# Performance work log

Measured on AMD Instinct MI355X. Metric: run time of the kernel, lower is better.

The kernel has to match this reference:

```python
import jax, jax.numpy as jnp
import numpy as np

B, T, V, E, H, FC, O = 4096, 64, 512, 32, 128, 256, 1024


def setup_inputs() -> dict:
    key = jax.random.key(0)
    ks = jax.random.split(key, 12)
    n = lambda k, shape, sc=1.0: (jax.random.normal(k, shape, jnp.float32) * sc)
    return {
        "message": n(ks[0], (B, T, V), 0.1),
        "W_emb": n(ks[1], (E, V), 0.05),
        "b_emb": n(ks[2], (E,), 0.05),
        "init_emb": n(ks[3], (1, 1, E), 1.0),
        "W_ih": n(ks[4], (3 * H, E), 0.08),
        "W_hh": n(ks[5], (3 * H, H), 0.08),
        "b_ih": n(ks[6], (3 * H,), 0.05),
        "b_hh": n(ks[7], (3 * H,), 0.05),
        "W_fc1": n(ks[8], (FC, H), 0.08),
        "b_fc1": n(ks[9], (FC,), 0.05),
        "W_fc2": n(ks[10], (O, FC), 0.05),
        "b_fc2": n(ks[11], (O,), 0.05),
    }


def reference(message, W_emb, b_emb, init_emb, W_ih, W_hh, b_ih, b_hh,
              W_fc1, b_fc1, W_fc2, b_fc2):
    Bb, Tt, Vv = message.shape
    Hh = W_hh.shape[1]
    # Per-step embedding of the message (torch does this inside the loop;
    # it is a pure per-timestep linear so we batch it once): [B,T,E]
    emb = jnp.einsum('btv,ev->bte', message, W_emb) + b_emb
    # Inputs consumed by the GRU at step t: initial_embedding at t=0,
    # then embedding(message[:, t-1]) for t >= 1. The embedding of the
    # final token is computed in torch but never fed to the GRU.
    x0 = jnp.broadcast_to(init_emb[0], (Bb, init_emb.shape[-1]))  # [B,E]
    xs = jnp.concatenate([x0[:, None, :], emb[:, :Tt - 1, :]], axis=1)  # [B,T,E]
    # Precompute input-side gate pre-activations for all steps: [T,B,3H]
    gi_all = jnp.einsum('bte,ge->tbg', xs, W_ih) + b_ih

    def gru_step(h, gi):
        gh = h @ W_hh.T + b_hh  # [B,3H]
        i_r, i_z, i_n = jnp.split(gi, 3, axis=-1)
        h_r, h_z, h_n = jnp.split(gh, 3, axis=-1)
        r = jax.nn.sigmoid(i_r + h_r)
        z = jax.nn.sigmoid(i_z + h_z)
        nng = jnp.tanh(i_n + r * h_n)
        h_new = (1.0 - z) * nng + z * h
        return h_new, None

    h0 = jnp.zeros((Bb, Hh), message.dtype)
    h_last, _ = jax.lax.scan(gru_step, h0, gi_all)
    hid = jax.nn.elu(h_last @ W_fc1.T + b_fc1)
    return jax.nn.sigmoid(hid @ W_fc2.T + b_fc2)
```

## Files before the change

### kernel.cpp

```cpp
#include <hip/hip_runtime.h>
#include <math.h>

#define B_ 4096
#define T_ 64
#define V_ 512
#define E_ 32
#define H_ 128
#define FC1_ 256
#define O_ 1024

typedef float f32x4 __attribute__((ext_vector_type(4)));
typedef short s16x8 __attribute__((ext_vector_type(8)));
typedef unsigned short u16;

#define MFMA16(a, b, c) __builtin_amdgcn_mfma_f32_16x16x32_bf16(a, b, c, 0, 0, 0)

union Frag { u16 q[8]; unsigned u[4]; s16x8 v; };

__device__ __forceinline__ u16 f2bf(float f) {
    union { float f; unsigned u; } v; v.f = f;
    unsigned r = v.u + 0x7FFFu + ((v.u >> 16) & 1u);
    return (u16)(r >> 16);
}
__device__ __forceinline__ unsigned cvtpk(float lo, float hi) {
    unsigned r;
    asm("v_cvt_pk_bf16_f32 %0, %1, %2" : "=v"(r) : "v"(lo), "v"(hi));
    return r;
}
__device__ __forceinline__ float sigf(float x) { return 1.0f / (1.0f + __expf(-x)); }
__device__ __forceinline__ float tanhfast(float x) {
    return 1.0f - 2.0f / (__expf(2.0f * x) + 1.0f);
}
__device__ __forceinline__ s16x8 gatherB(const float* W, int row, int K, int k0, int lh) {
    const float* p = W + (size_t)row * K + k0 + lh * 8;
    float4 a = *(const float4*)p;
    float4 b = *(const float4*)(p + 4);
    Frag f;
    f.u[0] = cvtpk(a.x, a.y); f.u[1] = cvtpk(a.z, a.w);
    f.u[2] = cvtpk(b.x, b.y); f.u[3] = cvtpk(b.z, b.w);
    return f.v;
}

#define LDS_BARRIER() do {                                         \
    asm volatile("s_waitcnt lgkmcnt(0)" ::: "memory");             \
    __builtin_amdgcn_s_barrier();                                  \
} while (0)

__global__ void __launch_bounds__(512, 2) fused_kernel(
    const float* __restrict__ msg,
    const float* __restrict__ Wemb, const float* __restrict__ b_emb,
    const float* __restrict__ init_emb,
    const float* __restrict__ Wih, const float* __restrict__ Whh,
    const float* __restrict__ b_ih, const float* __restrict__ b_hh,
    const float* __restrict__ Wfc1, const float* __restrict__ b_fc1,
    const float* __restrict__ Wfc2, const float* __restrict__ b_fc2,
    float* __restrict__ out) {
    __shared__ float mlds[2][16][516];
    __shared__ u16 hlds[2][16 * 136];
    __shared__ float epart[2][8][576];
    __shared__ u16 xfrag[2][640];
    u16* const hidl = (u16*)&epart[0][0][0];
    const int tid = threadIdx.x, w = tid >> 6, l = tid & 63;
    const int ln = l & 15, lh = l >> 4;
    const int wg = w & 3, wp = w >> 2;
    const int gb = blockIdx.x;

#define LOADCOL(BUF, C) do {                                                   \
    _Pragma("unroll")                                                          \
    for (int i_ = 0; i_ < 4; i_++) {                                           \
        int r_ = 2 * w + (i_ >> 1);                                            \
        int o_ = (i_ & 1) * 256 + l * 4;                                       \
        BUF[i_] = *(const f32x4*)(msg +                                        \
            ((size_t)(gb * 16 + r_) * T_ + (C)) * V_ + o_);                    \
    }                                                                          \
} while (0)
#define WRITECOL(BUF, MB) do {                                                 \
    _Pragma("unroll")                                                          \
    for (int i_ = 0; i_ < 4; i_++) {                                           \
        int r_ = 2 * w + (i_ >> 1);                                            \
        int o_ = (i_ & 1) * 256 + l * 4;                                       \
        *(f32x4*)&mlds[MB][r_][o_] = BUF[i_];                                  \
    }                                                                          \
} while (0)

    f32x4 mb0[4], mb1[4], mb2[4], mb3[4];
    LOADCOL(mb0, 0); LOADCOL(mb1, 1); LOADCOL(mb2, 2); LOADCOL(mb3, 3);

    s16x8 wh[3][4], wi[3], we[2][2];
    float br, bz, bin, bgn;
    {
        #pragma unroll
        for (int g = 0; g < 3; g++) {
            int gt = wg + 4 * wp + 8 * g;
            #pragma unroll
            for (int kc = 0; kc < 4; kc++)
                wh[g][kc] = gatherB(Whh, gt * 16 + ln, 128, kc * 32, lh);
            wi[g] = gatherB(Wih, gt * 16 + ln, 32, 0, lh);
        }
        #pragma unroll
        for (int kk = 0; kk < 2; kk++) {
            we[kk][0] = gatherB(Wemb, ln, 512, (2 * w + kk) * 32, lh);
            we[kk][1] = gatherB(Wemb, 16 + ln, 512, (2 * w + kk) * 32, lh);
        }
        int c = wg * 16 + wp * 64 + ln;
        br  = b_ih[c] + b_hh[c];
        bz  = b_ih[128 + c] + b_hh[128 + c];
        bin = b_ih[256 + c];
        bgn = b_hh[256 + c];
    }
    const float bev = b_emb[tid & 31];
    float hold[4] = {};

    for (int i = tid; i < 16 * 136; i += 512) hlds[0][i] = 0;
    {
        int fr_ = tid >> 5, fc_ = tid & 31;
        xfrag[1][fr_ * 40 + fc_] = f2bf(init_emb[fc_]);
    }
    WRITECOL(mb0, 0);
    WRITECOL(mb1, 1);
    __syncthreads();

#define EMBED_LDS(BUF, PAR) do {                                               \
    f32x4 e0 = {0.f, 0.f, 0.f, 0.f}, e1 = {0.f, 0.f, 0.f, 0.f};                \
    _Pragma("unroll")                                                          \
    for (int kk = 0; kk < 2; kk++) {                                           \
        const float* mp = &mlds[BUF][ln][(2 * w + kk) * 32 + lh * 8];          \
        f32x4 m0 = *(const f32x4*)mp;                                          \
        f32x4 m1 = *(const f32x4*)(mp + 4);                                    \
        Frag fa;                                                               \
        fa.u[0] = cvtpk(m0[0], m0[1]); fa.u[1] = cvtpk(m0[2], m0[3]);          \
        fa.u[2] = cvtpk(m1[0], m1[1]); fa.u[3] = cvtpk(m1[2], m1[3]);          \
        e0 = MFMA16(fa.v, we[kk][0], e0);                                      \
        e1 = MFMA16(fa.v, we[kk][1], e1);                                      \
    }                                                                          \
    _Pragma("unroll")                                                          \
    for (int i = 0; i < 4; i++) {                                              \
        epart[PAR][w][(lh * 4 + i) * 36 + ln]      = e0[i];                    \
        epart[PAR][w][(lh * 4 + i) * 36 + 16 + ln] = e1[i];                    \
    }                                                                          \
} while (0)

    EMBED_LDS(0, 1);
    LDS_BARRIER();

    const int aoff = ln * 136 + lh * 8;
    const int colo = wg * 16 + wp * 64 + ln;
    const int fr = tid >> 5, fc = tid & 31, fo = fr * 36 + fc;

#define GRU_STEP(TT, K, LOADF, WRF, EMBF, REDF, MB_L, MB_W) do {               \
    const int t = (TT);                                                        \
    if (LOADF) LOADCOL(MB_L, t + 4);                                           \
    const u16* hb = hlds[(K) & 1];                                             \
    s16x8 af0 = *(const s16x8*)(hb + aoff);                                    \
    s16x8 af1 = *(const s16x8*)(hb + aoff + 32);                               \
    s16x8 af2 = *(const s16x8*)(hb + aoff + 64);                               \
    s16x8 af3 = *(const s16x8*)(hb + aoff + 96);                               \
    s16x8 xc = *(const s16x8*)(&xfrag[((K) + 1) & 1][0] + ln * 40 + lh * 8);   \
    f32x4 ar  = {br, br, br, br};                                              \
    f32x4 az  = {bz, bz, bz, bz};                                              \
    f32x4 agn = {bgn, bgn, bgn, bgn};                                          \
    f32x4 ain = {bin, bin, bin, bin};                                          \
    ar  = MFMA16(xc, wi[0], ar);                                               \
    az  = MFMA16(xc, wi[1], az);                                               \
    ain = MFMA16(xc, wi[2], ain);                                              \
    ar  = MFMA16(af0, wh[0][0], ar);                                           \
    ar  = MFMA16(af1, wh[0][1], ar);                                           \
    ar  = MFMA16(af2, wh[0][2], ar);                                           \
    ar  = MFMA16(af3, wh[0][3], ar);                                           \
    az  = MFMA16(af0, wh[1][0], az);                                           \
    az  = MFMA16(af1, wh[1][1], az);                                           \
    az  = MFMA16(af2, wh[1][2], az);                                           \
    az  = MFMA16(af3, wh[1][3], az);                                           \
    agn = MFMA16(af0, wh[2][0], agn);                                          \
    agn = MFMA16(af1, wh[2][1], agn);                                          \
    agn = MFMA16(af2, wh[2][2], agn);                                          \
    agn = MFMA16(af3, wh[2][3], agn);                                          \
    if (WRF) WRITECOL(MB_W, (K) & 1);                                          \
    u16* hw = hlds[((K) + 1) & 1];                                             \
    float hn[4];                                                               \
    _Pragma("unroll")                                                          \
    for (int i = 0; i < 4; i++) {                                              \
        float rg = sigf(ar[i]);                                                \
        float zg = sigf(az[i]);                                                \
        float ng = tanhfast(ain[i] + rg * agn[i]);                             \
        hn[i] = zg * (hold[i] - ng) + ng;                                      \
        hold[i] = hn[i];                                                       \
    }                                                                          \
    {                                                                          \
        unsigned u01 = cvtpk(hn[0], hn[1]);                                    \
        unsigned u23 = cvtpk(hn[2], hn[3]);                                    \
        hw[(lh * 4 + 0) * 136 + colo] = (u16)(u01 & 0xFFFFu);                  \
        hw[(lh * 4 + 1) * 136 + colo] = (u16)(u01 >> 16);                      \
        hw[(lh * 4 + 2) * 136 + colo] = (u16)(u23 & 0xFFFFu);                  \
        hw[(lh * 4 + 3) * 136 + colo] = (u16)(u23 >> 16);                      \
    }                                                                          \
    if (EMBF) EMBED_LDS(((K) + 1) & 1, (K) & 1);                               \
    if (REDF) {                                                                \
        const float* eb = &epart[((K) + 1) & 1][0][0];                         \
        float s = eb[fo]           + eb[576 + fo]     + eb[2 * 576 + fo]       \
                + eb[3 * 576 + fo] + eb[4 * 576 + fo] + eb[5 * 576 + fo]       \
                + eb[6 * 576 + fo] + eb[7 * 576 + fo] + bev;                   \
        xfrag[(K) & 1][fr * 40 + fc] = f2bf(s);                                \
    }                                                                          \
    LDS_BARRIER();                                                             \
} while (0)

    for (int tt = 0; tt < 60; tt += 4) {
        GRU_STEP(tt + 0, 0, 1, 1, 1, 1, mb0, mb2);
        GRU_STEP(tt + 1, 1, 1, 1, 1, 1, mb1, mb3);
        GRU_STEP(tt + 2, 2, 1, 1, 1, 1, mb2, mb0);
        GRU_STEP(tt + 3, 3, 1, 1, 1, 1, mb3, mb1);
    }
    GRU_STEP(60, 0, 0, 1, 1, 1, mb0, mb2);
    GRU_STEP(61, 1, 0, 1, 1, 1, mb1, mb3);
    GRU_STEP(62, 2, 0, 0, 1, 1, mb2, mb0);
    GRU_STEP(63, 3, 0, 0, 0, 0, mb3, mb1);
#undef GRU_STEP
#undef LOADCOL
#undef WRITECOL
#undef EMBED_LDS

    const u16* hb = hlds[0];
    s16x8 hf0 = *(const s16x8*)(hb + aoff);
    s16x8 hf1 = *(const s16x8*)(hb + aoff + 32);
    s16x8 hf2 = *(const s16x8*)(hb + aoff + 64);
    s16x8 hf3 = *(const s16x8*)(hb + aoff + 96);
    #pragma unroll
    for (int q = 0; q < 2; q++) {
        int ot = 2 * w + q;
        float b1 = b_fc1[ot * 16 + ln];
        f32x4 a1 = {b1, b1, b1, b1};
        a1 = MFMA16(hf0, gatherB(Wfc1, ot * 16 + ln, 128, 0,  lh), a1);
        a1 = MFMA16(hf1, gatherB(Wfc1, ot * 16 + ln, 128, 32, lh), a1);
        a1 = MFMA16(hf2, gatherB(Wfc1, ot * 16 + ln, 128, 64, lh), a1);
        a1 = MFMA16(hf3, gatherB(Wfc1, ot * 16 + ln, 128, 96, lh), a1);
        #pragma unroll
        for (int i = 0; i < 4; i++) {
            float v = a1[i];
            v = v > 0.0f ? v : (__expf(v) - 1.0f);
            hidl[(lh * 4 + i) * 264 + ot * 16 + ln] = f2bf(v);
        }
    }
    LDS_BARRIER();

    s16x8 hf[8];
    #pragma unroll
    for (int kc = 0; kc < 8; kc++)
        hf[kc] = *(const s16x8*)(hidl + ln * 264 + kc * 32 + lh * 8);
    #pragma unroll
    for (int q = 0; q < 8; q++) {
        int nt = 8 * w + q;
        float b2 = b_fc2[nt * 16 + ln];
        f32x4 a2 = {b2, b2, b2, b2};
        #pragma unroll
        for (int kc = 0; kc < 8; kc++)
            a2 = MFMA16(hf[kc], gatherB(Wfc2, nt * 16 + ln, 256, kc * 32, lh), a2);
        #pragma unroll
        for (int i = 0; i < 4; i++)
            out[(size_t)(gb * 16 + lh * 4 + i) * 1024 + nt * 16 + ln] = sigf(a2[i]);
    }
}

extern "C" void kernel_launch(void* const* d_in, const int* in_sizes, int n_in,
                              void* d_out, int out_size, void* d_ws, size_t ws_size,
                              hipStream_t stream) {
    const float* message  = (const float*)d_in[0];
    const float* W_emb    = (const float*)d_in[1];
    const float* b_emb    = (const float*)d_in[2];
    const float* init_emb = (const float*)d_in[3];
    const float* W_ih     = (const float*)d_in[4];
    const float* W_hh     = (const float*)d_in[5];
    const float* b_ih     = (const float*)d_in[6];
    const float* b_hh     = (const float*)d_in[7];
    const float* W_fc1    = (const float*)d_in[8];
    const float* b_fc1    = (const float*)d_in[9];
    const float* W_fc2    = (const float*)d_in[10];
    const float* b_fc2    = (const float*)d_in[11];
    float* out = (float*)d_out;
    (void)d_ws; (void)ws_size;

    hipLaunchKernelGGL(fused_kernel, dim3(256), dim3(512), 0, stream,
                       message, W_emb, b_emb, init_emb, W_ih, W_hh, b_ih, b_hh,
                       W_fc1, b_fc1, W_fc2, b_fc2, out);
}
```

Before: 161.3 us.

## Specialize four extra wavefronts as message loaders feeding LDS for GRU waves

Raises the block to 768 threads and dedicates the four extra wavefronts to streaming message columns from global memory into the LDS double buffer, two steps ahead. The eight original wavefronts now only run the embedding, GRU recurrence and output MLP, so they no longer issue global loads or hold prefetch registers. The aim is to take global-load latency and register pressure off the serial recurrence path. In exchange, the prefetch depth drops from four columns to two, and the launch bound of (768, 3) may force heavy register limits and spills on the compute wavefronts.

```diff
diff --git a/kernel.cpp b/kernel.cpp
--- a/kernel.cpp
+++ b/kernel.cpp
@@ -46,7 +46,7 @@
     __builtin_amdgcn_s_barrier();                                  \
 } while (0)
 
-__global__ void __launch_bounds__(512, 2) fused_kernel(
+__global__ void __launch_bounds__(768, 3) fused_kernel(
     const float* __restrict__ msg,
     const float* __restrict__ Wemb, const float* __restrict__ b_emb,
     const float* __restrict__ init_emb,
@@ -62,33 +62,39 @@
     u16* const hidl = (u16*)&epart[0][0][0];
     const int tid = threadIdx.x, w = tid >> 6, l = tid & 63;
     const int ln = l & 15, lh = l >> 4;
-    const int wg = w & 3, wp = w >> 2;
+    const int wg = w & 3, wp = (w >> 2) & 1;
     const int gb = blockIdx.x;
-
-#define LOADCOL(BUF, C) do {                                                   \
-    _Pragma("unroll")                                                          \
-    for (int i_ = 0; i_ < 4; i_++) {                                           \
-        int r_ = 2 * w + (i_ >> 1);                                            \
+    const bool isload = (w >= 8);
+    const int lw = w & 3;
+
+#define L_LOAD(BUF, C) do {                                                    \
+    _Pragma("unroll")                                                          \
+    for (int i_ = 0; i_ < 8; i_++) {                                           \
+        int r_ = 4 * lw + (i_ >> 1);                                           \
         int o_ = (i_ & 1) * 256 + l * 4;                                       \
         BUF[i_] = *(const f32x4*)(msg +                                        \
             ((size_t)(gb * 16 + r_) * T_ + (C)) * V_ + o_);                    \
     }                                                                          \
 } while (0)
-#define WRITECOL(BUF, MB) do {                                                 \
-    _Pragma("unroll")                                                          \
-    for (int i_ = 0; i_ < 4; i_++) {                                           \
-        int r_ = 2 * w + (i_ >> 1);                                            \
+#define L_WRITE(BUF, MB) do {                                                  \
+    _Pragma("unroll")                                                          \
+    for (int i_ = 0; i_ < 8; i_++) {                                           \
+        int r_ = 4 * lw + (i_ >> 1);                                           \
         int o_ = (i_ & 1) * 256 + l * 4;                                       \
         *(f32x4*)&mlds[MB][r_][o_] = BUF[i_];                                  \
     }                                                                          \
 } while (0)
 
-    f32x4 mb0[4], mb1[4], mb2[4], mb3[4];
-    LOADCOL(mb0, 0); LOADCOL(mb1, 1); LOADCOL(mb2, 2); LOADCOL(mb3, 3);
-
+    f32x4 lb0[8], lb1[8];
     s16x8 wh[3][4], wi[3], we[2][2];
-    float br, bz, bin, bgn;
-    {
+    float br = 0.f, bz = 0.f, bin = 0.f, bgn = 0.f, bev = 0.f;
+    float hold[4] = {};
+
+    if (isload) {
+        L_LOAD(lb0, 0); L_WRITE(lb0, 0);
+        L_LOAD(lb1, 1); L_WRITE(lb1, 1);
+        L_LOAD(lb0, 2); L_LOAD(lb1, 3);
+    } else {
         #pragma unroll
         for (int g = 0; g < 3; g++) {
             int gt = wg + 4 * wp + 8 * g;
@@ -107,17 +113,13 @@
         bz  = b_ih[128 + c] + b_hh[128 + c];
         bin = b_ih[256 + c];
         bgn = b_hh[256 + c];
-    }
-    const float bev = b_emb[tid & 31];
-    float hold[4] = {};
-
-    for (int i = tid; i < 16 * 136; i += 512) hlds[0][i] = 0;
-    {
+        bev = b_emb[tid & 31];
+    }
+    if (tid < 512) {
+        for (int i = tid; i < 16 * 136; i += 512) hlds[0][i] = 0;
         int fr_ = tid >> 5, fc_ = tid & 31;
         xfrag[1][fr_ * 40 + fc_] = f2bf(init_emb[fc_]);
     }
-    WRITECOL(mb0, 0);
-    WRITECOL(mb1, 1);
     __syncthreads();
 
 #define EMBED_LDS(BUF, PAR) do {                                               \
@@ -140,124 +142,131 @@
     }                                                                          \
 } while (0)
 
-    EMBED_LDS(0, 1);
+    if (!isload) EMBED_LDS(0, 1);
     LDS_BARRIER();
 
     const int aoff = ln * 136 + lh * 8;
     const int colo = wg * 16 + wp * 64 + ln;
     const int fr = tid >> 5, fc = tid & 31, fo = fr * 36 + fc;
 
-#define GRU_STEP(TT, K, LOADF, WRF, EMBF, REDF, MB_L, MB_W) do {               \
+#define STEP(TT, P, LOADF, WRF, EMBF, REDF, LB) do {                           \
     const int t = (TT);                                                        \
-    if (LOADF) LOADCOL(MB_L, t + 4);                                           \
-    const u16* hb = hlds[(K) & 1];                                             \
-    s16x8 af0 = *(const s16x8*)(hb + aoff);                                    \
-    s16x8 af1 = *(const s16x8*)(hb + aoff + 32);                               \
-    s16x8 af2 = *(const s16x8*)(hb + aoff + 64);                               \
-    s16x8 af3 = *(const s16x8*)(hb + aoff + 96);                               \
-    s16x8 xc = *(const s16x8*)(&xfrag[((K) + 1) & 1][0] + ln * 40 + lh * 8);   \
-    f32x4 ar  = {br, br, br, br};                                              \
-    f32x4 az  = {bz, bz, bz, bz};                                              \
-    f32x4 agn = {bgn, bgn, bgn, bgn};                                          \
-    f32x4 ain = {bin, bin, bin, bin};                                          \
-    ar  = MFMA16(xc, wi[0], ar);                                               \
-    az  = MFMA16(xc, wi[1], az);                                               \
-    ain = MFMA16(xc, wi[2], ain);                                              \
-    ar  = MFMA16(af0, wh[0][0], ar);                                           \
-    ar  = MFMA16(af1, wh[0][1], ar);                                           \
-    ar  = MFMA16(af2, wh[0][2], ar);                                           \
-    ar  = MFMA16(af3, wh[0][3], ar);                                           \
-    az  = MFMA16(af0, wh[1][0], az);                                           \
-    az  = MFMA16(af1, wh[1][1], az);                                           \
-    az  = MFMA16(af2, wh[1][2], az);                                           \
-    az  = MFMA16(af3, wh[1][3], az);                                           \
-    agn = MFMA16(af0, wh[2][0], agn);                                          \
-    agn = MFMA16(af1, wh[2][1], agn);                                          \
-    agn = MFMA16(af2, wh[2][2], agn);                                          \
-    agn = MFMA16(af3, wh[2][3], agn);                                          \
-    if (WRF) WRITECOL(MB_W, (K) & 1);                                          \
-    u16* hw = hlds[((K) + 1) & 1];                                             \
-    float hn[4];                                                               \
-    _Pragma("unroll")                                                          \
-    for (int i = 0; i < 4; i++) {                                              \
-        float rg = sigf(ar[i]);                                                \
-        float zg = sigf(az[i]);                                                \
-        float ng = tanhfast(ain[i] + rg * agn[i]);                             \
-        hn[i] = zg * (hold[i] - ng) + ng;                                      \
-        hold[i] = hn[i];                                                       \
-    }                                                                          \
-    {                                                                          \
-        unsigned u01 = cvtpk(hn[0], hn[1]);                                    \
-        unsigned u23 = cvtpk(hn[2], hn[3]);                                    \
-        hw[(lh * 4 + 0) * 136 + colo] = (u16)(u01 & 0xFFFFu);                  \
-        hw[(lh * 4 + 1) * 136 + colo] = (u16)(u01 >> 16);                      \
-        hw[(lh * 4 + 2) * 136 + colo] = (u16)(u23 & 0xFFFFu);                  \
-        hw[(lh * 4 + 3) * 136 + colo] = (u16)(u23 >> 16);                      \
-    }                                                                          \
-    if (EMBF) EMBED_LDS(((K) + 1) & 1, (K) & 1);                               \
-    if (REDF) {                                                                \
-        const float* eb = &epart[((K) + 1) & 1][0][0];                         \
-        float s = eb[fo]           + eb[576 + fo]     + eb[2 * 576 + fo]       \
-                + eb[3 * 576 + fo] + eb[4 * 576 + fo] + eb[5 * 576 + fo]       \
-                + eb[6 * 576 + fo] + eb[7 * 576 + fo] + bev;                   \
-        xfrag[(K) & 1][fr * 40 + fc] = f2bf(s);                                \
+    if (isload) {                                                              \
+        if (WRF) L_WRITE(LB, (P));                                             \
+        if (LOADF) L_LOAD(LB, t + 4);                                          \
+    } else {                                                                   \
+        const u16* hb = hlds[(P)];                                             \
+        s16x8 af0 = *(const s16x8*)(hb + aoff);                                \
+        s16x8 af1 = *(const s16x8*)(hb + aoff + 32);                           \
+        s16x8 af2 = *(const s16x8*)(hb + aoff + 64);                           \
+        s16x8 af3 = *(const s16x8*)(hb + aoff + 96);                           \
+        s16x8 xc = *(const s16x8*)(&xfrag[1 - (P)][0] + ln * 40 + lh * 8);     \
+        f32x4 ar  = {br, br, br, br};                                          \
+        f32x4 az  = {bz, bz, bz, bz};                                          \
+        f32x4 agn = {bgn, bgn, bgn, bgn};                                      \
+        f32x4 ain = {bin, bin, bin, bin};                                      \
+        ar  = MFMA16(xc, wi[0], ar);                                           \
+        az  = MFMA16(xc, wi[1], az);                                           \
+        ain = MFMA16(xc, wi[2], ain);                                          \
+        ar  = MFMA16(af0, wh[0][0], ar);                                       \
+        ar  = MFMA16(af1, wh[0][1], ar);                                       \
+        ar  = MFMA16(af2, wh[0][2], ar);                                       \
+        ar  = MFMA16(af3, wh[0][3], ar);                                       \
+        az  = MFMA16(af0, wh[1][0], az);                                       \
+        az  = MFMA16(af1, wh[1][1], az);                                       \
+        az  = MFMA16(af2, wh[1][2], az);                                       \
+        az  = MFMA16(af3, wh[1][3], az);                                       \
+        agn = MFMA16(af0, wh[2][0], agn);                                      \
+        agn = MFMA16(af1, wh[2][1], agn);                                      \
+        agn = MFMA16(af2, wh[2][2], agn);                                      \
+        agn = MFMA16(af3, wh[2][3], agn);                                      \
+        u16* hw = hlds[1 - (P)];                                               \
+        float hn[4];                                                           \
+        _Pragma("unroll")                                                      \
+        for (int i = 0; i < 4; i++) {                                          \
+            float rg = sigf(ar[i]);                                            \
+            float zg = sigf(az[i]);                                            \
+            float ng = tanhfast(ain[i] + rg * agn[i]);                         \
+            hn[i] = zg * (hold[i] - ng) + ng;                                  \
+            hold[i] = hn[i];                                                   \
+        }                                                                      \
+        {                                                                      \
+            unsigned u01 = cvtpk(hn[0], hn[1]);                                \
+            unsigned u23 = cvtpk(hn[2], hn[3]);                                \
+            hw[(lh * 4 + 0) * 136 + colo] = (u16)(u01 & 0xFFFFu);              \
+            hw[(lh * 4 + 1) * 136 + colo] = (u16)(u01 >> 16);                  \
+            hw[(lh * 4 + 2) * 136 + colo] = (u16)(u23 & 0xFFFFu);              \
+            hw[(lh * 4 + 3) * 136 + colo] = (u16)(u23 >> 16);                  \
+        }                                                                      \
+        if (EMBF) EMBED_LDS(1 - (P), (P));                                     \
+        if (REDF) {                                                            \
+            const float* eb = &epart[1 - (P)][0][0];                           \
+            float s = eb[fo]           + eb[576 + fo]     + eb[2 * 576 + fo]   \
+                    + eb[3 * 576 + fo] + eb[4 * 576 + fo] + eb[5 * 576 + fo]   \
+                    + eb[6 * 576 + fo] + eb[7 * 576 + fo] + bev;               \
+            xfrag[(P)][fr * 40 + fc] = f2bf(s);                                \
+        }                                                                      \
     }                                                                          \
     LDS_BARRIER();                                                             \
 } while (0)
 
-    for (int tt = 0; tt < 60; tt += 4) {
-        GRU_STEP(tt + 0, 0, 1, 1, 1, 1, mb0, mb2);
-        GRU_STEP(tt + 1, 1, 1, 1, 1, 1, mb1, mb3);
-        GRU_STEP(tt + 2, 2, 1, 1, 1, 1, mb2, mb0);
-        GRU_STEP(tt + 3, 3, 1, 1, 1, 1, mb3, mb1);
-    }
-    GRU_STEP(60, 0, 0, 1, 1, 1, mb0, mb2);
-    GRU_STEP(61, 1, 0, 1, 1, 1, mb1, mb3);
-    GRU_STEP(62, 2, 0, 0, 1, 1, mb2, mb0);
-    GRU_STEP(63, 3, 0, 0, 0, 0, mb3, mb1);
-#undef GRU_STEP
-#undef LOADCOL
-#undef WRITECOL
+    for (int tt = 0; tt < 58; tt += 2) {
+        STEP(tt + 0, 0, 1, 1, 1, 1, lb0);
+        STEP(tt + 1, 1, 1, 1, 1, 1, lb1);
+    }
+    STEP(58, 0, 1, 1, 1, 1, lb0);
+    STEP(59, 1, 0, 1, 1, 1, lb1);
+    STEP(60, 0, 0, 1, 1, 1, lb0);
+    STEP(61, 1, 0, 0, 1, 1, lb1);
+    STEP(62, 0, 0, 0, 0, 1, lb0);
+    STEP(63, 1, 0, 0, 0, 0, lb1);
+#undef STEP
+#undef L_LOAD
+#undef L_WRITE
 #undef EMBED_LDS
 
-    const u16* hb = hlds[0];
-    s16x8 hf0 = *(const s16x8*)(hb + aoff);
-    s16x8 hf1 = *(const s16x8*)(hb + aoff + 32);
-    s16x8 hf2 = *(const s16x8*)(hb + aoff + 64);
-    s16x8 hf3 = *(const s16x8*)(hb + aoff + 96);
-    #pragma unroll
-    for (int q = 0; q < 2; q++) {
-        int ot = 2 * w + q;
-        float b1 = b_fc1[ot * 16 + ln];
-        f32x4 a1 = {b1, b1, b1, b1};
-        a1 = MFMA16(hf0, gatherB(Wfc1, ot * 16 + ln, 128, 0,  lh), a1);
-        a1 = MFMA16(hf1, gatherB(Wfc1, ot * 16 + ln, 128, 32, lh), a1);
-        a1 = MFMA16(hf2, gatherB(Wfc1, ot * 16 + ln, 128, 64, lh), a1);
-        a1 = MFMA16(hf3, gatherB(Wfc1, ot * 16 + ln, 128, 96, lh), a1);
-        #pragma unroll
-        for (int i = 0; i < 4; i++) {
-            float v = a1[i];
-            v = v > 0.0f ? v : (__expf(v) - 1.0f);
-            hidl[(lh * 4 + i) * 264 + ot * 16 + ln] = f2bf(v);
+    if (!isload) {
+        const u16* hb = hlds[0];
+        s16x8 hf0 = *(const s16x8*)(hb + aoff);
+        s16x8 hf1 = *(const s16x8*)(hb + aoff + 32);
+        s16x8 hf2 = *(const s16x8*)(hb + aoff + 64);
+        s16x8 hf3 = *(const s16x8*)(hb + aoff + 96);
+        #pragma unroll
+        for (int q = 0; q < 2; q++) {
+            int ot = 2 * w + q;
+            float b1 = b_fc1[ot * 16 + ln];
+            f32x4 a1 = {b1, b1, b1, b1};
+            a1 = MFMA16(hf0, gatherB(Wfc1, ot * 16 + ln, 128, 0,  lh), a1);
+            a1 = MFMA16(hf1, gatherB(Wfc1, ot * 16 + ln, 128, 32, lh), a1);
+            a1 = MFMA16(hf2, gatherB(Wfc1, ot * 16 + ln, 128, 64, lh), a1);
+            a1 = MFMA16(hf3, gatherB(Wfc1, ot * 16 + ln, 128, 96, lh), a1);
+            #pragma unroll
+            for (int i = 0; i < 4; i++) {
+                float v = a1[i];
+                v = v > 0.0f ? v : (__expf(v) - 1.0f);
+                hidl[(lh * 4 + i) * 264 + ot * 16 + ln] = f2bf(v);
+            }
         }
     }
     LDS_BARRIER();
 
-    s16x8 hf[8];
-    #pragma unroll
-    for (int kc = 0; kc < 8; kc++)
-        hf[kc] = *(const s16x8*)(hidl + ln * 264 + kc * 32 + lh * 8);
-    #pragma unroll
-    for (int q = 0; q < 8; q++) {
-        int nt = 8 * w + q;
-        float b2 = b_fc2[nt * 16 + ln];
-        f32x4 a2 = {b2, b2, b2, b2};
+    if (!isload) {
+        s16x8 hf[8];
         #pragma unroll
         for (int kc = 0; kc < 8; kc++)
-            a2 = MFMA16(hf[kc], gatherB(Wfc2, nt * 16 + ln, 256, kc * 32, lh), a2);
-        #pragma unroll
-        for (int i = 0; i < 4; i++)
-            out[(size_t)(gb * 16 + lh * 4 + i) * 1024 + nt * 16 + ln] = sigf(a2[i]);
+            hf[kc] = *(const s16x8*)(hidl + ln * 264 + kc * 32 + lh * 8);
+        #pragma unroll
+        for (int q = 0; q < 8; q++) {
+            int nt = 8 * w + q;
+            float b2 = b_fc2[nt * 16 + ln];
+            f32x4 a2 = {b2, b2, b2, b2};
+            #pragma unroll
+            for (int kc = 0; kc < 8; kc++)
+                a2 = MFMA16(hf[kc], gatherB(Wfc2, nt * 16 + ln, 256, kc * 32, lh), a2);
+            #pragma unroll
+            for (int i = 0; i < 4; i++)
+                out[(size_t)(gb * 16 + lh * 4 + i) * 1024 + nt * 16 + ln] = sigf(a2[i]);
+        }
     }
 }
 
@@ -279,7 +288,7 @@
     float* out = (float*)d_out;
     (void)d_ws; (void)ws_size;
 
-    hipLaunchKernelGGL(fused_kernel, dim3(256), dim3(512), 0, stream,
+    hipLaunchKernelGGL(fused_kernel, dim3(256), dim3(768), 0, stream,
                        message, W_emb, b_emb, init_emb, W_ih, W_hh, b_ih, b_hh,
                        W_fc1, b_fc1, W_fc2, b_fc2, out);
 }
```

Result: slower. 361.1 us (+123.9%).
